# Kernel tuning notes

Hardware: AMD Instinct MI355X
Metric: run time of the kernel (lower is better)

## Reference

```python
import jax, jax.numpy as jnp
import numpy as np


def _shift_kernel(dtype=jnp.float32):
    # IdealDelayKernels: 9 output channels, 8 one-hot 3x3 shift taps (center skipped), 9th all-zero
    k = np.zeros((9, 1, 1, 3, 3), np.float32)
    idx = -1
    for i in range(3):
        for j in range(3):
            if i == 1 and j == 1:
                continue
            idx += 1
            k[idx, 0, 0, i, j] = 1.0
    return jnp.asarray(k, dtype)


def _conv2d(x, w, b, pad):
    y = jax.lax.conv_general_dilated(x, w, (1, 1), [(pad, pad), (pad, pad)],
                                     dimension_numbers=('NCHW', 'OIHW', 'NCHW'))
    return y if b is None else y + b[None, :, None, None]


def setup_inputs() -> dict:
    key = jax.random.key(0)
    ks = jax.random.split(key, 16)
    B, C, H, W = 2, 19, 512, 512
    s = 0.1  # xavier-ish scale for small convs
    return {
        'x': jax.random.normal(ks[0], (B, C, H, W), jnp.float32),
        'image': jax.random.normal(ks[1], (B, 3, H, W), jnp.float32),
        # IntraNetwork(3 -> 16 -> 16 -> 19): conv3x3, conv3x3, conv1x1 (BN frozen at identity)
        'intra_w1': jax.random.normal(ks[2], (16, 3, 3, 3), jnp.float32) * s,
        'intra_b1': jnp.zeros((16,), jnp.float32),
        'intra_w2': jax.random.normal(ks[3], (16, 16, 3, 3), jnp.float32) * s,
        'intra_b2': jnp.zeros((16,), jnp.float32),
        'intra_w3': jax.random.normal(ks[4], (19, 16, 1, 1), jnp.float32) * s,
        'intra_b3': jnp.zeros((19,), jnp.float32),
        # GuidingNetwork(20 -> 32 -> 32 -> 11): conv3x3, conv3x3, conv1x1 + sigmoid
        'guide_w1': jax.random.normal(ks[5], (32, 20, 3, 3), jnp.float32) * s,
        'guide_b1': jnp.zeros((32,), jnp.float32),
        'guide_w2': jax.random.normal(ks[6], (32, 32, 3, 3), jnp.float32) * s,
        'guide_b2': jnp.zeros((32,), jnp.float32),
        'guide_w3': jax.random.normal(ks[7], (11, 32, 1, 1), jnp.float32) * s,
        'guide_b3': jnp.zeros((11,), jnp.float32),
    }


def reference(x, image, intra_w1, intra_b1, intra_w2, intra_b2, intra_w3, intra_b3,
              guide_w1, guide_b1, guide_w2, guide_b2, guide_w3, guide_b3):
    # intra_net: image -> [B,19,H,W] (frozen BN == identity)
    f = jax.nn.relu(_conv2d(image, intra_w1, intra_b1, 1))
    f = jax.nn.relu(_conv2d(f, intra_w2, intra_b2, 1))
    intra = _conv2d(f, intra_w3, intra_b3, 0)            # [B,19,H,W]

    # Laplacian edge on the argmax label map
    single_x = jnp.argmax(x, axis=1, keepdims=True).astype(x.dtype)  # [B,1,H,W]
    lapla = jnp.full((1, 1, 3, 3), 1.0, x.dtype).at[0, 0, 1, 1].set(-8.0)
    edge = _conv2d(single_x, lapla, None, 1)             # [B,1,H,W]

    # guiding network: cat(intra, edge) -> 11 per-pixel guide weights
    gi = jnp.concatenate([intra, edge], axis=1)          # [B,20,H,W]
    g = jax.nn.relu(_conv2d(gi, guide_w1, guide_b1, 1))
    g = jax.nn.relu(_conv2d(g, guide_w2, guide_b2, 1))
    g = jax.nn.sigmoid(_conv2d(g, guide_w3, guide_b3, 0))  # [B,11,H,W]
    guide_feat = g[:, :, None]                           # [B,11,1,H,W]
    guide_feat = guide_feat / (jnp.sum(guide_feat, axis=1, keepdims=True) + 1e-9)

    # shift-kernel conv3d: [B,1,19,H,W] -> [B,9,19,H,W]
    xs = x[:, None]
    short = jax.lax.conv_general_dilated(xs, _shift_kernel(x.dtype), (1, 1, 1),
                                         [(0, 0), (1, 1), (1, 1)],
                                         dimension_numbers=('NCDHW', 'OIDHW', 'NCDHW'))
    xcat = jnp.concatenate([xs, short, intra[:, None]], axis=1)  # [B,11,19,H,W]

    out = jnp.sum(guide_feat * xcat, axis=1)             # [B,19,H,W]
    return (out, guide_feat, edge)
```

## Files before the change

kernel.cpp:

```cpp
#include <hip/hip_runtime.h>
#include <math.h>

constexpr int H = 512, W = 512, B = 2;
constexpr int HW = H * W;

typedef __attribute__((ext_vector_type(8))) short short8;
typedef __attribute__((ext_vector_type(4))) float floatx4;
typedef __attribute__((ext_vector_type(4))) unsigned int uint4v;

__device__ inline unsigned short f2bf(float f) {
  union { float f; unsigned int u; } x{f};
  const unsigned int u = x.u;
  return (unsigned short)((u + 0x7FFFu + ((u >> 16) & 1u)) >> 16);
}
__device__ inline float bf2f(unsigned short s) {
  union { unsigned int u; float f; } x;
  x.u = (unsigned int)s << 16;
  return x.f;
}
__device__ inline void unpk2(unsigned int u, float& lo, float& hi) {
  union { unsigned int u; float f; } a, b;
  a.u = u << 16;
  b.u = u & 0xffff0000u;
  lo = a.f;
  hi = b.f;
}

__device__ inline void load_row3(const float* __restrict__ plane, int hh,
                                 int w, float r[3]) {
  r[0] = 0.f; r[1] = 0.f; r[2] = 0.f;
  if ((unsigned)hh < (unsigned)H) {
    const float* rp = plane + (size_t)hh * W + w;
    r[1] = rp[0];
    if (w > 0) r[0] = rp[-1];
    if (w + 1 < W) r[2] = rp[1];
  }
}

template <int CIN, int COUT, bool RELU>
__global__ __launch_bounds__(256) void conv3x3_fp32_pack(
    const float* __restrict__ in0, const float* __restrict__ wgt,
    const float* __restrict__ bias, unsigned short* __restrict__ outp) {
  constexpr int TS = 16, TH = 18, LDW = 20;
  __shared__ float tile[CIN][TH][LDW];
  const int tx = threadIdx.x, ty = threadIdx.y;
  const int tid = ty * 16 + tx;
  const int w0 = blockIdx.x * TS, h0 = blockIdx.y * TS, b = blockIdx.z;

  for (int idx = tid; idx < CIN * TH * TH; idx += 256) {
    const int cin = idx / (TH * TH);
    const int rem = idx - cin * (TH * TH);
    const int r = rem / TH, c = rem - r * TH;
    const int gh = h0 + r - 1, gw = w0 + c - 1;
    float v = 0.f;
    if ((unsigned)gh < (unsigned)H && (unsigned)gw < (unsigned)W)
      v = in0[(size_t)(b * CIN + cin) * HW + gh * W + gw];
    tile[cin][r][c] = v;
  }
  __syncthreads();

  float acc[COUT];
#pragma unroll
  for (int co = 0; co < COUT; ++co) acc[co] = bias[co];
  for (int cin = 0; cin < CIN; ++cin) {
#pragma unroll
    for (int t = 0; t < 9; ++t) {
      const int ky = t / 3, kx = t - ky * 3;
      const float v = tile[cin][ty + ky][tx + kx];
#pragma unroll
      for (int co = 0; co < COUT; ++co)
        acc[co] = fmaf(v, wgt[(co * CIN + cin) * 9 + t], acc[co]);
    }
  }
  const int oh = h0 + ty, ow = w0 + tx;
  unsigned int pk[COUT / 2];
#pragma unroll
  for (int c2 = 0; c2 < COUT / 2; ++c2) {
    float a0 = acc[2 * c2], a1 = acc[2 * c2 + 1];
    if (RELU) { a0 = fmaxf(a0, 0.f); a1 = fmaxf(a1, 0.f); }
    pk[c2] = (unsigned)f2bf(a0) | ((unsigned)f2bf(a1) << 16);
  }
  unsigned short* dst = outp + ((size_t)(b * H + oh) * W + ow) * COUT;
#pragma unroll
  for (int u = 0; u < COUT / 8; ++u)
    *(uint4v*)(dst + u * 8) = uint4v{pk[u * 4], pk[u * 4 + 1], pk[u * 4 + 2], pk[u * 4 + 3]};
}

template <int CIN, int CINP, int COUT, int KS>
__global__ __launch_bounds__(256) void repack_w(
    const float* __restrict__ w, unsigned short* __restrict__ bp) {
  constexpr int NT = COUT / 16;
  const int idx = blockIdx.x * 256 + threadIdx.x;
  if (idx >= NT * KS * 512) return;
  const int j = idx & 7;
  const int l = (idx >> 3) & 63;
  const int ks = (idx >> 9) % KS;
  const int nt = idx / (KS * 512);
  const int co = nt * 16 + (l & 15);
  const int kglob = ks * 32 + (l >> 4) * 8 + j;
  const int tap = kglob / CINP;
  const int cin = kglob % CINP;
  float v = 0.f;
  if (tap < 9 && cin < CIN) v = w[((size_t)co * CIN + cin) * 9 + tap];
  bp[idx] = f2bf(v);
}

template <int CINP, int KS, int NT, bool EDGE19, int EPI>
__global__ __launch_bounds__(256) void conv3x3_mfma(
    const unsigned short* __restrict__ inp, const float* __restrict__ edg,
    const unsigned short* __restrict__ bpack, const float* __restrict__ bias,
    const float* __restrict__ ew, const float* __restrict__ eb,
    unsigned short* __restrict__ outp, float* __restrict__ outf,
    const float* __restrict__ xin, const unsigned short* __restrict__ ipn,
    float* __restrict__ outc) {
  constexpr int COUT = NT * 16;
  constexpr int CS = (CINP == 16) ? 24 : 40;
  constexpr int EPS = (EPI == 1) ? 24 : 40;
  constexpr int TR = 10;
  __shared__ __align__(16) unsigned short tile[TR * 34 * CS];

  const int tid = threadIdx.x;
  const int w0 = blockIdx.x * 32, h0 = blockIdx.y * 8, b = blockIdx.z;

  for (int idx = tid; idx < TR * 34; idx += 256) {
    const int r = idx / 34, c = idx - r * 34;
    const int gh = h0 + r - 1, gw = w0 + c - 1;
    unsigned short* dst = tile + (size_t)(r * 34 + c) * CS;
    if ((unsigned)gh < (unsigned)H && (unsigned)gw < (unsigned)W) {
      const unsigned short* src = inp + ((size_t)(b * H + gh) * W + gw) * CINP;
#pragma unroll
      for (int u = 0; u < CINP / 8; ++u)
        *(uint4v*)(dst + u * 8) = *(const uint4v*)(src + u * 8);
      if (EDGE19) dst[19] = f2bf(edg[(size_t)b * HW + gh * W + gw]);
    } else {
#pragma unroll
      for (int u = 0; u < CINP / 8; ++u)
        *(uint4v*)(dst + u * 8) = uint4v{0, 0, 0, 0};
    }
  }
  __syncthreads();

  const int wv = tid >> 6, lane = tid & 63;
  const int q = lane >> 4, l15 = lane & 15;
  const int rb = wv * 2;

  floatx4 acc[4][NT];
#pragma unroll
  for (int mf = 0; mf < 4; ++mf)
#pragma unroll
    for (int nt = 0; nt < NT; ++nt) acc[mf][nt] = floatx4{0.f, 0.f, 0.f, 0.f};

#pragma unroll
  for (int ks = 0; ks < KS; ++ks) {
    short8 bfrag[NT];
#pragma unroll
    for (int nt = 0; nt < NT; ++nt)
      bfrag[nt] = *(const short8*)(bpack + (size_t)(((nt * KS) + ks) * 64 + lane) * 8);

    const int kbase = ks * 32;
    const int kq = kbase + q * 8;
    int tapq = kq / CINP;
    const int cinq = kq % CINP;
    if (tapq > 8) tapq = 8;
    const int ky = tapq / 3, kx = tapq - ky * 3;
    const unsigned short* aptr =
        tile + (size_t)((rb + ky) * 34 + (l15 + kx)) * CS + cinq;

#pragma unroll
    for (int mf = 0; mf < 4; ++mf) {
      constexpr int mfs[4][2] = {{0, 0}, {0, 16}, {1, 0}, {1, 16}};
      const int off = (mfs[mf][0] * 34 + mfs[mf][1]) * CS;
      const short8 af = *(const short8*)(aptr + off);
#pragma unroll
      for (int nt = 0; nt < NT; ++nt)
        acc[mf][nt] = __builtin_amdgcn_mfma_f32_16x16x32_bf16(
            af, bfrag[nt], acc[mf][nt], 0, 0, 0);
    }
  }

  if constexpr (EPI == 0) {
#pragma unroll
    for (int nt = 0; nt < NT; ++nt) {
      const float bv = bias[nt * 16 + l15];
#pragma unroll
      for (int mf = 0; mf < 4; ++mf) {
        const int row = mf >> 1, colb = (mf & 1) * 16 + q * 4;
        unsigned short* dst =
            outp + ((size_t)(b * H + h0 + rb + row) * W + w0) * COUT + nt * 16 + l15;
#pragma unroll
        for (int rg = 0; rg < 4; ++rg) {
          const float v = fmaxf(acc[mf][nt][rg] + bv, 0.f);
          dst[(size_t)(colb + rg) * COUT] = f2bf(v);
        }
      }
    }
  } else {
    __syncthreads();
#pragma unroll
    for (int nt = 0; nt < NT; ++nt) {
      const float bv = bias[nt * 16 + l15];
#pragma unroll
      for (int mf = 0; mf < 4; ++mf) {
        const int row = rb + (mf >> 1), colb = (mf & 1) * 16 + q * 4;
#pragma unroll
        for (int rg = 0; rg < 4; ++rg) {
          const int px = row * 32 + colb + rg;
          tile[(size_t)px * EPS + nt * 16 + l15] =
              f2bf(fmaxf(acc[mf][nt][rg] + bv, 0.f));
        }
      }
    }
    __syncthreads();

    {
      const int p = tid;
      const int gh = h0 + (p >> 5), gw = w0 + (p & 31);
      const unsigned short* src = tile + (size_t)p * EPS;

      if constexpr (EPI == 1) {
        float xi[16];
        const uint4v r0 = *(const uint4v*)src;
        const uint4v r1 = *(const uint4v*)(src + 8);
        unpk2(r0.x, xi[0], xi[1]);   unpk2(r0.y, xi[2], xi[3]);
        unpk2(r0.z, xi[4], xi[5]);   unpk2(r0.w, xi[6], xi[7]);
        unpk2(r1.x, xi[8], xi[9]);   unpk2(r1.y, xi[10], xi[11]);
        unpk2(r1.z, xi[12], xi[13]); unpk2(r1.w, xi[14], xi[15]);
        float a[19];
#pragma unroll
        for (int co = 0; co < 19; ++co) a[co] = eb[co];
#pragma unroll
        for (int c = 0; c < 16; ++c) {
          const float v = xi[c];
#pragma unroll
          for (int co = 0; co < 19; ++co) a[co] = fmaf(v, ew[co * 16 + c], a[co]);
        }
        unsigned int pk[12];
#pragma unroll
        for (int j = 0; j < 9; ++j)
          pk[j] = (unsigned)f2bf(a[2 * j]) | ((unsigned)f2bf(a[2 * j + 1]) << 16);
        pk[9] = (unsigned)f2bf(a[18]);
        pk[10] = 0; pk[11] = 0;
        unsigned short* dst = outp + ((size_t)(b * H + gh) * W + gw) * 24;
#pragma unroll
        for (int u = 0; u < 3; ++u)
          *(uint4v*)(dst + u * 8) =
              uint4v{pk[u * 4], pk[u * 4 + 1], pk[u * 4 + 2], pk[u * 4 + 3]};
      } else {
        float xi[32];
#pragma unroll
        for (int u = 0; u < 4; ++u) {
          const uint4v r = *(const uint4v*)(src + u * 8);
          unpk2(r.x, xi[u * 8 + 0], xi[u * 8 + 1]);
          unpk2(r.y, xi[u * 8 + 2], xi[u * 8 + 3]);
          unpk2(r.z, xi[u * 8 + 4], xi[u * 8 + 5]);
          unpk2(r.w, xi[u * 8 + 6], xi[u * 8 + 7]);
        }
        float g[11], sum = 0.f;
#pragma unroll
        for (int co = 0; co < 11; ++co) {
          float a = eb[co];
#pragma unroll
          for (int c = 0; c < 32; ++c) a = fmaf(xi[c], ew[co * 32 + c], a);
          g[co] = 1.f / (1.f + expf(-a));
          sum += g[co];
        }
        const float inv = 1.f / (sum + 1e-9f);
        const size_t s = (size_t)gh * W + gw;
#pragma unroll
        for (int co = 0; co < 11; ++co)
          outf[(size_t)(b * 11 + co) * HW + s] = g[co] * inv;

        if constexpr (EPI == 3) {
          float gn[11];
#pragma unroll
          for (int m = 0; m < 11; ++m) gn[m] = g[m] * inv;
          const unsigned short* ip = ipn + ((size_t)b * HW + s) * 24;
          for (int c = 0; c < 19; ++c) {
            const float* xc = xin + (size_t)(b * 19 + c) * HW;
            float r0[3], r1[3], r2[3];
            load_row3(xc, gh - 1, gw, r0);
            load_row3(xc, gh, gw, r1);
            load_row3(xc, gh + 1, gw, r2);
            const float itv = bf2f(ip[c]);
            float a = gn[0] * r1[1];
            a = fmaf(gn[1], r0[0], a);
            a = fmaf(gn[2], r0[1], a);
            a = fmaf(gn[3], r0[2], a);
            a = fmaf(gn[4], r1[0], a);
            a = fmaf(gn[5], r1[2], a);
            a = fmaf(gn[6], r2[0], a);
            a = fmaf(gn[7], r2[1], a);
            a = fmaf(gn[8], r2[2], a);
            a = fmaf(gn[10], itv, a);
            outc[(size_t)(b * 19 + c) * HW + s] = a;
          }
        }
      }
    }
  }
}

__global__ __launch_bounds__(256) void argmax_kernel(
    const float* __restrict__ x, float* __restrict__ sx) {
  const int t = blockIdx.x * 256 + threadIdx.x;
  const int b = t >> 18;
  const int s = t & (HW - 1);
  const float* xp = x + (size_t)b * 19 * HW + s;
  float bv = *xp;
  float ix = 0.f;
#pragma unroll
  for (int c = 1; c < 19; ++c) {
    const float v = xp[(size_t)c * HW];
    if (v > bv) { bv = v; ix = (float)c; }
  }
  sx[(size_t)b * HW + s] = ix;
}

__device__ inline void load_row4(const float* __restrict__ plane, int hh,
                                 int w0, float r[4]) {
#pragma unroll
  for (int i = 0; i < 4; ++i) r[i] = 0.f;
  if ((unsigned)hh < (unsigned)H) {
    const float* rp = plane + (size_t)hh * W + w0;
    const float2 m = *(const float2*)rp;
    r[1] = m.x; r[2] = m.y;
    if (w0 > 0) r[0] = rp[-1];
    if (w0 + 2 < W) r[3] = rp[2];
  }
}

__global__ __launch_bounds__(256) void edge_kernel(
    const float* __restrict__ sx, float* __restrict__ edge) {
  const int t = blockIdx.x * 256 + threadIdx.x;
  const int b = t / (HW / 2);
  const int s2 = (t - b * (HW / 2)) * 2;
  const int h = s2 / W, w0 = s2 - h * W;
  const float* sp = sx + (size_t)b * HW;
  float r0[4], r1[4], r2[4];
  load_row4(sp, h - 1, w0, r0);
  load_row4(sp, h, w0, r1);
  load_row4(sp, h + 1, w0, r2);
  float o[2];
#pragma unroll
  for (int k = 0; k < 2; ++k)
    o[k] = r0[k] + r0[k + 1] + r0[k + 2] + r1[k] + r1[k + 2] + r2[k] +
           r2[k + 1] + r2[k + 2] - 8.f * r1[k + 1];
  *(float2*)(edge + (size_t)b * HW + s2) = float2{o[0], o[1]};
}

extern "C" void kernel_launch(void* const* d_in, const int* in_sizes, int n_in,
                              void* d_out, int out_size, void* d_ws,
                              size_t ws_size, hipStream_t stream) {
  const float* x     = (const float*)d_in[0];
  const float* image = (const float*)d_in[1];
  const float* iw1 = (const float*)d_in[2];
  const float* ib1 = (const float*)d_in[3];
  const float* iw2 = (const float*)d_in[4];
  const float* ib2 = (const float*)d_in[5];
  const float* iw3 = (const float*)d_in[6];
  const float* ib3 = (const float*)d_in[7];
  const float* gw1 = (const float*)d_in[8];
  const float* gb1 = (const float*)d_in[9];
  const float* gw2 = (const float*)d_in[10];
  const float* gb2 = (const float*)d_in[11];
  const float* gw3 = (const float*)d_in[12];
  const float* gb3 = (const float*)d_in[13];

  float* ws = (float*)d_ws;
  float* sx = ws;
  unsigned short* f1p  = (unsigned short*)(ws + (size_t)2 * HW);
  unsigned short* intp = (unsigned short*)(ws + (size_t)34 * HW);
  unsigned short* g1p  = (unsigned short*)(ws + (size_t)58 * HW);
  unsigned short* bp_ic2 = (unsigned short*)(ws + (size_t)122 * HW);
  unsigned short* bp_gc1 = bp_ic2 + 4096;
  unsigned short* bp_gc2 = bp_gc1 + 12288;

  float* out0 = (float*)d_out;
  float* gfo  = out0 + (size_t)2 * 19 * HW;
  float* edg  = gfo + (size_t)2 * 11 * HW;

  const dim3 blk16(16, 16);
  const dim3 grd16(W / 16, H / 16, B);
  const dim3 grdM(W / 32, H / 8, B);
  const int flat1 = (B * HW) / 256;
  const int flat2 = (B * HW / 2) / 256;

  argmax_kernel<<<flat1, 256, 0, stream>>>(x, sx);
  edge_kernel<<<flat2, 256, 0, stream>>>(sx, edg);

  repack_w<16, 16, 16, 5><<<10, 256, 0, stream>>>(iw2, bp_ic2);
  repack_w<20, 24, 32, 7><<<28, 256, 0, stream>>>(gw1, bp_gc1);
  repack_w<32, 32, 32, 9><<<36, 256, 0, stream>>>(gw2, bp_gc2);

  conv3x3_fp32_pack<3, 16, true><<<grd16, blk16, 0, stream>>>(image, iw1, ib1, f1p);
  conv3x3_mfma<16, 5, 1, false, 1><<<grdM, 256, 0, stream>>>(
      f1p, nullptr, bp_ic2, ib2, iw3, ib3, intp, nullptr, nullptr, nullptr, nullptr);
  conv3x3_mfma<24, 7, 2, true, 0><<<grdM, 256, 0, stream>>>(
      intp, edg, bp_gc1, gb1, nullptr, nullptr, g1p, nullptr, nullptr, nullptr, nullptr);
  conv3x3_mfma<32, 9, 2, false, 3><<<grdM, 256, 0, stream>>>(
      g1p, nullptr, bp_gc2, gb2, gw3, gb3, nullptr, gfo, x, intp, out0);
}
```

Measured before the change: 237.8 us.

## Fuse Laplacian edge into guide conv1 tile load and merge weight repacks

The standalone edge kernel is removed. The first guiding-network conv now computes the 3x3 Laplacian from the argmax map while it loads its input tile, and writes the edge output from there. The three weight-repack launches are also merged into one kernel that dispatches on block index. This removes launches and one pass over the edge map, at the cost of redundant stencil loads on halo pixels and duplicate edge writes from overlapping tiles.

```diff
diff --git a/kernel.cpp b/kernel.cpp
--- a/kernel.cpp
+++ b/kernel.cpp
@@ -87,10 +87,9 @@
 }
 
 template <int CIN, int CINP, int COUT, int KS>
-__global__ __launch_bounds__(256) void repack_w(
-    const float* __restrict__ w, unsigned short* __restrict__ bp) {
+__device__ inline void repack_body(int idx, const float* __restrict__ w,
+                                   unsigned short* __restrict__ bp) {
   constexpr int NT = COUT / 16;
-  const int idx = blockIdx.x * 256 + threadIdx.x;
   if (idx >= NT * KS * 512) return;
   const int j = idx & 7;
   const int l = (idx >> 3) & 63;
@@ -103,6 +102,20 @@
   float v = 0.f;
   if (tap < 9 && cin < CIN) v = w[((size_t)co * CIN + cin) * 9 + tap];
   bp[idx] = f2bf(v);
+}
+
+__global__ __launch_bounds__(256) void repack_all(
+    const float* __restrict__ iw2, const float* __restrict__ gw1,
+    const float* __restrict__ gw2, unsigned short* __restrict__ bp_ic2,
+    unsigned short* __restrict__ bp_gc1, unsigned short* __restrict__ bp_gc2) {
+  const int blk = blockIdx.x, tid = threadIdx.x;
+  if (blk < 10) {
+    repack_body<16, 16, 16, 5>(blk * 256 + tid, iw2, bp_ic2);
+  } else if (blk < 38) {
+    repack_body<20, 24, 32, 7>((blk - 10) * 256 + tid, gw1, bp_gc1);
+  } else {
+    repack_body<32, 32, 32, 9>((blk - 38) * 256 + tid, gw2, bp_gc2);
+  }
 }
 
 template <int CINP, int KS, int NT, bool EDGE19, int EPI>
@@ -131,7 +144,17 @@
 #pragma unroll
       for (int u = 0; u < CINP / 8; ++u)
         *(uint4v*)(dst + u * 8) = *(const uint4v*)(src + u * 8);
-      if (EDGE19) dst[19] = f2bf(edg[(size_t)b * HW + gh * W + gw]);
+      if (EDGE19) {
+        const float* sp = edg + (size_t)b * HW;
+        float r0[3], r1[3], r2[3];
+        load_row3(sp, gh - 1, gw, r0);
+        load_row3(sp, gh, gw, r1);
+        load_row3(sp, gh + 1, gw, r2);
+        const float e = r0[0] + r0[1] + r0[2] + r1[0] + r1[2] + r2[0] +
+                        r2[1] + r2[2] - 8.f * r1[1];
+        dst[19] = f2bf(e);
+        outf[(size_t)b * HW + (size_t)gh * W + gw] = e;
+      }
     } else {
 #pragma unroll
       for (int u = 0; u < CINP / 8; ++u)
@@ -316,38 +339,6 @@
   sx[(size_t)b * HW + s] = ix;
 }
 
-__device__ inline void load_row4(const float* __restrict__ plane, int hh,
-                                 int w0, float r[4]) {
-#pragma unroll
-  for (int i = 0; i < 4; ++i) r[i] = 0.f;
-  if ((unsigned)hh < (unsigned)H) {
-    const float* rp = plane + (size_t)hh * W + w0;
-    const float2 m = *(const float2*)rp;
-    r[1] = m.x; r[2] = m.y;
-    if (w0 > 0) r[0] = rp[-1];
-    if (w0 + 2 < W) r[3] = rp[2];
-  }
-}
-
-__global__ __launch_bounds__(256) void edge_kernel(
-    const float* __restrict__ sx, float* __restrict__ edge) {
-  const int t = blockIdx.x * 256 + threadIdx.x;
-  const int b = t / (HW / 2);
-  const int s2 = (t - b * (HW / 2)) * 2;
-  const int h = s2 / W, w0 = s2 - h * W;
-  const float* sp = sx + (size_t)b * HW;
-  float r0[4], r1[4], r2[4];
-  load_row4(sp, h - 1, w0, r0);
-  load_row4(sp, h, w0, r1);
-  load_row4(sp, h + 1, w0, r2);
-  float o[2];
-#pragma unroll
-  for (int k = 0; k < 2; ++k)
-    o[k] = r0[k] + r0[k + 1] + r0[k + 2] + r1[k] + r1[k + 2] + r2[k] +
-           r2[k + 1] + r2[k + 2] - 8.f * r1[k + 1];
-  *(float2*)(edge + (size_t)b * HW + s2) = float2{o[0], o[1]};
-}
-
 extern "C" void kernel_launch(void* const* d_in, const int* in_sizes, int n_in,
                               void* d_out, int out_size, void* d_ws,
                               size_t ws_size, hipStream_t stream) {
@@ -383,20 +374,15 @@
   const dim3 grd16(W / 16, H / 16, B);
   const dim3 grdM(W / 32, H / 8, B);
   const int flat1 = (B * HW) / 256;
-  const int flat2 = (B * HW / 2) / 256;
 
   argmax_kernel<<<flat1, 256, 0, stream>>>(x, sx);
-  edge_kernel<<<flat2, 256, 0, stream>>>(sx, edg);
-
-  repack_w<16, 16, 16, 5><<<10, 256, 0, stream>>>(iw2, bp_ic2);
-  repack_w<20, 24, 32, 7><<<28, 256, 0, stream>>>(gw1, bp_gc1);
-  repack_w<32, 32, 32, 9><<<36, 256, 0, stream>>>(gw2, bp_gc2);
+  repack_all<<<74, 256, 0, stream>>>(iw2, gw1, gw2, bp_ic2, bp_gc1, bp_gc2);
 
   conv3x3_fp32_pack<3, 16, true><<<grd16, blk16, 0, stream>>>(image, iw1, ib1, f1p);
   conv3x3_mfma<16, 5, 1, false, 1><<<grdM, 256, 0, stream>>>(
       f1p, nullptr, bp_ic2, ib2, iw3, ib3, intp, nullptr, nullptr, nullptr, nullptr);
   conv3x3_mfma<24, 7, 2, true, 0><<<grdM, 256, 0, stream>>>(
-      intp, edg, bp_gc1, gb1, nullptr, nullptr, g1p, nullptr, nullptr, nullptr, nullptr);
+      intp, sx, bp_gc1, gb1, nullptr, nullptr, g1p, edg, nullptr, nullptr, nullptr);
   conv3x3_mfma<32, 9, 2, false, 3><<<grdM, 256, 0, stream>>>(
       g1p, nullptr, bp_gc2, gb2, gw3, gb3, nullptr, gfo, x, intp, out0);
 }
```

After: 228.8 us. 1.04x faster.
